# Kernel optimization log

Measured on AMD Instinct MI355X. Metric: run time of the kernel, lower is better.

Reference implementation:

```python
import jax, jax.numpy as jnp
import numpy as np

B, N, M, HW = 8, 256, 32, 32768
W_CLASS, W_CENTER, W_MASK, W_DICE = 2.0, 1.0, 5.0, 2.0


def setup_inputs() -> dict:
    key = jax.random.key(0)
    ks = jax.random.split(key, 6)
    sem_cls_prob = jax.random.uniform(ks[0], (B, N, 1), dtype=jnp.float32)
    center_dist = jax.random.uniform(ks[1], (B, N, M), dtype=jnp.float32)
    mask_heatmaps = jax.random.normal(ks[2], (B, HW, N), dtype=jnp.float32)
    # binary targets, as assumed by the dice/BCE cost math
    mask_tgt = jnp.round(jax.random.uniform(ks[3], (B, M, HW), dtype=jnp.float32))
    gt_plane_sem_cls_label = jax.random.randint(ks[4], (B, M), 0, 2).astype(jnp.int64)
    nactual_gt = jax.random.randint(ks[5], (B,), 1, M + 1).astype(jnp.int64)
    return {
        'sem_cls_prob': sem_cls_prob,
        'center_dist': center_dist,
        'mask_heatmaps': mask_heatmaps,
        'mask_tgt': mask_tgt,
        'gt_plane_sem_cls_label': gt_plane_sem_cls_label,
        'nactual_gt': nactual_gt,
    }


def _final_cost(sem_cls_prob, center_dist, mask_heatmaps, mask_tgt, labels):
    # class cost: -gathered prob from cat(1-p, p) -> [B, N, M]
    cls_cat = jnp.concatenate([1.0 - sem_cls_prob, sem_cls_prob], axis=-1)  # [B, N, 2]
    lbl = jnp.broadcast_to(labels[:, None, :], (B, N, M))
    class_mat = -jnp.take_along_axis(cls_cat, lbl, axis=2)

    x = jnp.swapaxes(mask_heatmaps, 1, 2)  # [B, N, HW] logits (mask_heatmaps[b].T)
    # BCE-with-logits: pos = softplus(-x) (target=1), neg = x + softplus(-x) (target=0)
    pos = jax.nn.softplus(-x)
    neg = x + pos
    cost_mask = (jnp.einsum('bnc,bmc->bnm', pos, mask_tgt)
                 + jnp.einsum('bnc,bmc->bnm', neg, 1.0 - mask_tgt)) / HW

    s = jax.nn.sigmoid(x)
    numerator = 2.0 * jnp.einsum('bnc,bmc->bnm', s, mask_tgt)
    denominator = s.sum(-1)[:, :, None] + mask_tgt.sum(-1)[:, None, :]
    cost_dice = 1.0 - (numerator + 1.0) / (denominator + 1.0)

    return (W_CLASS * class_mat + W_CENTER * center_dist
            + W_MASK * cost_mask + W_DICE * cost_dice)


def reference(sem_cls_prob, center_dist, mask_heatmaps, mask_tgt,
              gt_plane_sem_cls_label, nactual_gt):
    # nactual_gt only gates the (serial, CPU) Hungarian step, which is out of
    # kernel scope; the GPU-side math is the fused final cost matrix.
    return _final_cost(sem_cls_prob, center_dist, mask_heatmaps, mask_tgt,
                       gt_plane_sem_cls_label)
```

## Files before the change

### kernel.cpp

```cpp
#include <hip/hip_runtime.h>
#include <hip/hip_bf16.h>

#define NB   8
#define NN   256
#define NM   32
#define NHW  32768

#define CCH    4
#define CSLAB  (NHW / CCH)
#define NT     16
#define WPB    8
#define CW     (CSLAB / WPB)
#define ITERS  (CW / 32)

#define OFF_DXP  0
#define SZ_DXP   (CCH*NB*NT*512)
#define OFF_DSP  (OFF_DXP + SZ_DXP)
#define SZ_DSP   SZ_DXP
#define OFF_SNP  (OFF_DSP + SZ_DSP)
#define SZ_SNP   (CCH*NB*NN)
#define OFF_SSP  (OFF_SNP + SZ_SNP)
#define SZ_SSP   SZ_SNP
#define OFF_STGT (OFF_SSP + SZ_SSP)

typedef _Float16 half8 __attribute__((ext_vector_type(8)));
typedef float    f32x4 __attribute__((ext_vector_type(4)));

__global__ __launch_bounds__(256) void sum_tgt(const float* __restrict__ T,
                                               float* __restrict__ ws) {
    const int blk  = blockIdx.x;
    const int tid  = threadIdx.x;
    const int lane = tid & 63;
    const int wave = tid >> 6;
    const float* tp = T + (size_t)blk * NHW;

    float s = 0.f;
    for (int k = 0; k < NHW / (256 * 4); ++k) {
        float4 v = *(const float4*)(tp + (size_t)k * 1024 + tid * 4);
        s += (v.x + v.y) + (v.z + v.w);
    }
    s += __shfl_down(s, 32);
    s += __shfl_down(s, 16);
    s += __shfl_down(s, 8);
    s += __shfl_down(s, 4);
    s += __shfl_down(s, 2);
    s += __shfl_down(s, 1);

    __shared__ float r4[4];
    if (lane == 0) r4[wave] = s;
    __syncthreads();
    if (tid == 0) ws[OFF_STGT + blk] = (r4[0] + r4[1]) + (r4[2] + r4[3]);
}

__global__ __launch_bounds__(512, 4) void cost_main(
    const float* __restrict__ X,
    const float* __restrict__ T,
    float* __restrict__ ws) {
    const int blk  = blockIdx.x;
    const int b    = blk & 7;
    const int rest = blk >> 3;
    const int ch   = rest & 3;
    const int nt   = rest >> 2;

    const int tid  = threadIdx.x;
    const int wave = tid >> 6;
    const int lane = tid & 63;
    const int l16  = lane & 15;
    const int quad = lane >> 4;

    const int n0 = nt * 16;
    const int c0 = ch * CSLAB + wave * CW;

    const float* Xp  = X + ((size_t)b * NHW + c0 + quad * 8) * NN + n0 + l16;
    const float* T0p = T + ((size_t)b * NM + l16)      * NHW + c0 + quad * 8;
    const float* T1p = T + ((size_t)b * NM + l16 + 16) * NHW + c0 + quad * 8;

    f32x4 ax0 = {0.f, 0.f, 0.f, 0.f}, ax1 = {0.f, 0.f, 0.f, 0.f};
    f32x4 as0 = {0.f, 0.f, 0.f, 0.f}, as1 = {0.f, 0.f, 0.f, 0.f};
    float sneg = 0.f, ssig = 0.f;

    for (int it = 0; it < ITERS; ++it) {
        float xv[8];
#pragma unroll
        for (int j = 0; j < 8; ++j)
            xv[j] = Xp[(size_t)j * NN];

        float4 ta = *(const float4*)(T0p);
        float4 tb = *(const float4*)(T0p + 4);
        float4 tc = *(const float4*)(T1p);
        float4 td = *(const float4*)(T1p + 4);

        half8 hx, hs, ht0, ht1;
#pragma unroll
        for (int j = 0; j < 8; ++j) {
            float x = xv[j];
            float e = __expf(-fabsf(x));
            float r = __builtin_amdgcn_rcpf(1.f + e);
            float s = (x >= 0.f) ? r : 1.f - r;
            float pos = fmaxf(-x, 0.f) + __logf(1.f + e);
            sneg += x + pos;
            ssig += s;
            hx[j] = (_Float16)x;
            hs[j] = (_Float16)s;
        }
        ht0[0] = (_Float16)ta.x; ht0[1] = (_Float16)ta.y;
        ht0[2] = (_Float16)ta.z; ht0[3] = (_Float16)ta.w;
        ht0[4] = (_Float16)tb.x; ht0[5] = (_Float16)tb.y;
        ht0[6] = (_Float16)tb.z; ht0[7] = (_Float16)tb.w;
        ht1[0] = (_Float16)tc.x; ht1[1] = (_Float16)tc.y;
        ht1[2] = (_Float16)tc.z; ht1[3] = (_Float16)tc.w;
        ht1[4] = (_Float16)td.x; ht1[5] = (_Float16)td.y;
        ht1[6] = (_Float16)td.z; ht1[7] = (_Float16)td.w;

        ax0 = __builtin_amdgcn_mfma_f32_16x16x32_f16(hx, ht0, ax0, 0, 0, 0);
        ax1 = __builtin_amdgcn_mfma_f32_16x16x32_f16(hx, ht1, ax1, 0, 0, 0);
        as0 = __builtin_amdgcn_mfma_f32_16x16x32_f16(hs, ht0, as0, 0, 0, 0);
        as1 = __builtin_amdgcn_mfma_f32_16x16x32_f16(hs, ht1, as1, 0, 0, 0);

        Xp  += (size_t)32 * NN;
        T0p += 32;
        T1p += 32;
    }

    __shared__ float redx[512];
    __shared__ float reds[512];
    __shared__ float redn[16];
    __shared__ float redss[16];
    redx[tid] = 0.f;
    reds[tid] = 0.f;
    if (tid < 16) { redn[tid] = 0.f; redss[tid] = 0.f; }
    __syncthreads();

#pragma unroll
    for (int r = 0; r < 4; ++r) {
        const int row = quad * 4 + r;
        atomicAdd(&redx[row * 32 + l16],      ax0[r]);
        atomicAdd(&redx[row * 32 + l16 + 16], ax1[r]);
        atomicAdd(&reds[row * 32 + l16],      as0[r]);
        atomicAdd(&reds[row * 32 + l16 + 16], as1[r]);
    }
    sneg += __shfl_down(sneg, 32);
    sneg += __shfl_down(sneg, 16);
    ssig += __shfl_down(ssig, 32);
    ssig += __shfl_down(ssig, 16);
    if (lane < 16) {
        atomicAdd(&redn[l16], sneg);
        atomicAdd(&redss[l16], ssig);
    }
    __syncthreads();

    const size_t base = ((size_t)(ch * NB + b) * NT + nt);
    ws[OFF_DXP + base * 512 + tid] = redx[tid];
    ws[OFF_DSP + base * 512 + tid] = reds[tid];
    if (tid < 16) {
        ws[OFF_SNP + (ch * NB + b) * NN + n0 + tid] = redn[tid];
        ws[OFF_SSP + (ch * NB + b) * NN + n0 + tid] = redss[tid];
    }
}

__global__ __launch_bounds__(256) void cost_finalize(
    const float* __restrict__ P,
    const float* __restrict__ CD,
    const int*   __restrict__ LAB,
    const float* __restrict__ ws,
    float* __restrict__ out) {
    const int idx = blockIdx.x * 256 + threadIdx.x;
    const int m = idx & 31;
    const int n = (idx >> 5) & 255;
    const int b = idx >> 13;
    const int nt = n >> 4, nl = n & 15;

    float dx = 0.f, ds = 0.f, sn = 0.f, ss = 0.f;
#pragma unroll
    for (int ch = 0; ch < CCH; ++ch) {
        const size_t base = ((size_t)(ch * NB + b) * NT + nt) * 512 + nl * 32 + m;
        dx += ws[OFF_DXP + base];
        ds += ws[OFF_DSP + base];
        sn += ws[OFF_SNP + (ch * NB + b) * NN + n];
        ss += ws[OFF_SSP + (ch * NB + b) * NN + n];
    }
    const float st  = ws[OFF_STGT + b * NM + m];
    const float p   = P[b * NN + n];
    const int   lab = LAB[b * NM + m];
    const float cls = lab ? -p : (p - 1.f);

    const float cmask = (sn - dx) * (1.f / (float)NHW);
    const float dice  = 1.f - (2.f * ds + 1.f) / (ss + st + 1.f);

    out[idx] = 2.f * cls + CD[idx] + 5.f * cmask + 2.f * dice;
}

extern "C" void kernel_launch(void* const* d_in, const int* in_sizes, int n_in,
                              void* d_out, int out_size, void* d_ws, size_t ws_size,
                              hipStream_t stream) {
    const float* P   = (const float*)d_in[0];
    const float* CD  = (const float*)d_in[1];
    const float* X   = (const float*)d_in[2];
    const float* T   = (const float*)d_in[3];
    const int*   LAB = (const int*)d_in[4];
    float* out = (float*)d_out;
    float* ws  = (float*)d_ws;

    hipLaunchKernelGGL(sum_tgt, dim3(NB * NM), dim3(256), 0, stream, T, ws);
    hipLaunchKernelGGL(cost_main, dim3(NB * NT * CCH), dim3(512), 0, stream, X, T, ws);
    hipLaunchKernelGGL(cost_finalize, dim3((NB * NN * NM) / 256), dim3(256), 0, stream,
                       P, CD, LAB, ws, out);
}
```

Measured before the change: 433.6 us.

## Widen N tile to 64 to reuse target fragments and fuse target sum

Each block now covers 64 prediction rows instead of 16, so the converted target fragments are loaded once and reused across four MFMA column groups rather than re-read by sixteen separate N-tiles. The HW dimension is split into 16 chunks instead of 4 to keep the block count at 512. The separate target-sum kernel is removed and its row sums are computed inside the main loop, with the finalize kernel adding the per-chunk partials. The cost is more accumulator registers per thread, larger shared-memory reductions, and more partials for the finalize kernel to read.

After: 529.7 us. 22.2% more time.

```diff
diff --git a/kernel.cpp b/kernel.cpp
--- a/kernel.cpp
+++ b/kernel.cpp
@@ -6,61 +6,35 @@
 #define NM   32
 #define NHW  32768
 
-#define CCH    4
+#define NT4    4
+#define CCH    16
 #define CSLAB  (NHW / CCH)
-#define NT     16
 #define WPB    8
 #define CW     (CSLAB / WPB)
-#define ITERS  (CW / 32)
+#define KSTEPS (CW / 32)
 
 #define OFF_DXP  0
-#define SZ_DXP   (CCH*NB*NT*512)
+#define SZ_DXP   (CCH*NB*NT4*2048)
 #define OFF_DSP  (OFF_DXP + SZ_DXP)
-#define SZ_DSP   SZ_DXP
-#define OFF_SNP  (OFF_DSP + SZ_DSP)
+#define OFF_SNP  (OFF_DSP + SZ_DXP)
 #define SZ_SNP   (CCH*NB*NN)
 #define OFF_SSP  (OFF_SNP + SZ_SNP)
-#define SZ_SSP   SZ_SNP
-#define OFF_STGT (OFF_SSP + SZ_SSP)
+#define OFF_STGT (OFF_SSP + SZ_SNP)
 
 typedef _Float16 half8 __attribute__((ext_vector_type(8)));
 typedef float    f32x4 __attribute__((ext_vector_type(4)));
 
-__global__ __launch_bounds__(256) void sum_tgt(const float* __restrict__ T,
-                                               float* __restrict__ ws) {
-    const int blk  = blockIdx.x;
-    const int tid  = threadIdx.x;
-    const int lane = tid & 63;
-    const int wave = tid >> 6;
-    const float* tp = T + (size_t)blk * NHW;
-
-    float s = 0.f;
-    for (int k = 0; k < NHW / (256 * 4); ++k) {
-        float4 v = *(const float4*)(tp + (size_t)k * 1024 + tid * 4);
-        s += (v.x + v.y) + (v.z + v.w);
-    }
-    s += __shfl_down(s, 32);
-    s += __shfl_down(s, 16);
-    s += __shfl_down(s, 8);
-    s += __shfl_down(s, 4);
-    s += __shfl_down(s, 2);
-    s += __shfl_down(s, 1);
-
-    __shared__ float r4[4];
-    if (lane == 0) r4[wave] = s;
-    __syncthreads();
-    if (tid == 0) ws[OFF_STGT + blk] = (r4[0] + r4[1]) + (r4[2] + r4[3]);
-}
+#define MFMA16(a, b, c) __builtin_amdgcn_mfma_f32_16x16x32_f16(a, b, c, 0, 0, 0)
 
 __global__ __launch_bounds__(512, 4) void cost_main(
     const float* __restrict__ X,
     const float* __restrict__ T,
     float* __restrict__ ws) {
-    const int blk  = blockIdx.x;
-    const int b    = blk & 7;
-    const int rest = blk >> 3;
-    const int ch   = rest & 3;
-    const int nt   = rest >> 2;
+    const int blk = blockIdx.x;
+    const int b   = blk & 7;
+    const int rr  = blk >> 3;
+    const int ch  = rr & (CCH - 1);
+    const int nt4 = rr >> 4;
 
     const int tid  = threadIdx.x;
     const int wave = tid >> 6;
@@ -68,94 +42,117 @@
     const int l16  = lane & 15;
     const int quad = lane >> 4;
 
-    const int n0 = nt * 16;
+    const int n0 = nt4 * 64;
     const int c0 = ch * CSLAB + wave * CW;
 
     const float* Xp  = X + ((size_t)b * NHW + c0 + quad * 8) * NN + n0 + l16;
-    const float* T0p = T + ((size_t)b * NM + l16)      * NHW + c0 + quad * 8;
-    const float* T1p = T + ((size_t)b * NM + l16 + 16) * NHW + c0 + quad * 8;
-
-    f32x4 ax0 = {0.f, 0.f, 0.f, 0.f}, ax1 = {0.f, 0.f, 0.f, 0.f};
-    f32x4 as0 = {0.f, 0.f, 0.f, 0.f}, as1 = {0.f, 0.f, 0.f, 0.f};
-    float sneg = 0.f, ssig = 0.f;
-
-    for (int it = 0; it < ITERS; ++it) {
-        float xv[8];
-#pragma unroll
-        for (int j = 0; j < 8; ++j)
-            xv[j] = Xp[(size_t)j * NN];
-
+    const float* T0p = T + ((size_t)b * NM + l16) * NHW + c0 + quad * 8;
+    const float* T1p = T0p + (size_t)16 * NHW;
+
+    f32x4 ax0[4], ax1[4], as0[4], as1[4];
+#pragma unroll
+    for (int f = 0; f < 4; ++f) {
+        ax0[f] = f32x4{0.f, 0.f, 0.f, 0.f};
+        ax1[f] = f32x4{0.f, 0.f, 0.f, 0.f};
+        as0[f] = f32x4{0.f, 0.f, 0.f, 0.f};
+        as1[f] = f32x4{0.f, 0.f, 0.f, 0.f};
+    }
+    float sneg[4] = {0.f, 0.f, 0.f, 0.f};
+    float ssig[4] = {0.f, 0.f, 0.f, 0.f};
+    float ts0 = 0.f, ts1 = 0.f;
+
+    for (int ks = 0; ks < KSTEPS; ++ks) {
         float4 ta = *(const float4*)(T0p);
         float4 tb = *(const float4*)(T0p + 4);
         float4 tc = *(const float4*)(T1p);
         float4 td = *(const float4*)(T1p + 4);
-
-        half8 hx, hs, ht0, ht1;
-#pragma unroll
-        for (int j = 0; j < 8; ++j) {
-            float x = xv[j];
-            float e = __expf(-fabsf(x));
-            float r = __builtin_amdgcn_rcpf(1.f + e);
-            float s = (x >= 0.f) ? r : 1.f - r;
-            float pos = fmaxf(-x, 0.f) + __logf(1.f + e);
-            sneg += x + pos;
-            ssig += s;
-            hx[j] = (_Float16)x;
-            hs[j] = (_Float16)s;
-        }
-        ht0[0] = (_Float16)ta.x; ht0[1] = (_Float16)ta.y;
-        ht0[2] = (_Float16)ta.z; ht0[3] = (_Float16)ta.w;
-        ht0[4] = (_Float16)tb.x; ht0[5] = (_Float16)tb.y;
-        ht0[6] = (_Float16)tb.z; ht0[7] = (_Float16)tb.w;
-        ht1[0] = (_Float16)tc.x; ht1[1] = (_Float16)tc.y;
-        ht1[2] = (_Float16)tc.z; ht1[3] = (_Float16)tc.w;
-        ht1[4] = (_Float16)td.x; ht1[5] = (_Float16)td.y;
-        ht1[6] = (_Float16)td.z; ht1[7] = (_Float16)td.w;
-
-        ax0 = __builtin_amdgcn_mfma_f32_16x16x32_f16(hx, ht0, ax0, 0, 0, 0);
-        ax1 = __builtin_amdgcn_mfma_f32_16x16x32_f16(hx, ht1, ax1, 0, 0, 0);
-        as0 = __builtin_amdgcn_mfma_f32_16x16x32_f16(hs, ht0, as0, 0, 0, 0);
-        as1 = __builtin_amdgcn_mfma_f32_16x16x32_f16(hs, ht1, as1, 0, 0, 0);
-
+        half8 ht0 = {(_Float16)ta.x, (_Float16)ta.y, (_Float16)ta.z, (_Float16)ta.w,
+                     (_Float16)tb.x, (_Float16)tb.y, (_Float16)tb.z, (_Float16)tb.w};
+        half8 ht1 = {(_Float16)tc.x, (_Float16)tc.y, (_Float16)tc.z, (_Float16)tc.w,
+                     (_Float16)td.x, (_Float16)td.y, (_Float16)td.z, (_Float16)td.w};
+        ts0 += (ta.x + ta.y) + (ta.z + ta.w) + (tb.x + tb.y) + (tb.z + tb.w);
+        ts1 += (tc.x + tc.y) + (tc.z + tc.w) + (td.x + td.y) + (td.z + td.w);
+
+#pragma unroll
+        for (int f = 0; f < 4; ++f) {
+            float xv[8];
+#pragma unroll
+            for (int j = 0; j < 8; ++j)
+                xv[j] = Xp[(size_t)j * NN + f * 16];
+            half8 hx, hs;
+#pragma unroll
+            for (int j = 0; j < 8; ++j) {
+                float x = xv[j];
+                float e = __expf(-fabsf(x));
+                float rc = __builtin_amdgcn_rcpf(1.f + e);
+                float s  = (x >= 0.f) ? rc : 1.f - rc;
+                float pos = fmaxf(-x, 0.f) + __logf(1.f + e);
+                sneg[f] += x + pos;
+                ssig[f] += s;
+                hx[j] = (_Float16)x;
+                hs[j] = (_Float16)s;
+            }
+            ax0[f] = MFMA16(hx, ht0, ax0[f]);
+            ax1[f] = MFMA16(hx, ht1, ax1[f]);
+            as0[f] = MFMA16(hs, ht0, as0[f]);
+            as1[f] = MFMA16(hs, ht1, as1[f]);
+        }
         Xp  += (size_t)32 * NN;
         T0p += 32;
         T1p += 32;
     }
 
-    __shared__ float redx[512];
-    __shared__ float reds[512];
-    __shared__ float redn[16];
-    __shared__ float redss[16];
-    redx[tid] = 0.f;
-    reds[tid] = 0.f;
-    if (tid < 16) { redn[tid] = 0.f; redss[tid] = 0.f; }
+    __shared__ float redx[2048];
+    __shared__ float reds[2048];
+    __shared__ float redn[64];
+    __shared__ float redss[64];
+    __shared__ float redt[32];
+    for (int i = tid; i < 2048; i += 512) { redx[i] = 0.f; reds[i] = 0.f; }
+    if (tid < 64) { redn[tid] = 0.f; redss[tid] = 0.f; }
+    if (tid < 32) redt[tid] = 0.f;
     __syncthreads();
 
 #pragma unroll
-    for (int r = 0; r < 4; ++r) {
-        const int row = quad * 4 + r;
-        atomicAdd(&redx[row * 32 + l16],      ax0[r]);
-        atomicAdd(&redx[row * 32 + l16 + 16], ax1[r]);
-        atomicAdd(&reds[row * 32 + l16],      as0[r]);
-        atomicAdd(&reds[row * 32 + l16 + 16], as1[r]);
-    }
-    sneg += __shfl_down(sneg, 32);
-    sneg += __shfl_down(sneg, 16);
-    ssig += __shfl_down(ssig, 32);
-    ssig += __shfl_down(ssig, 16);
-    if (lane < 16) {
-        atomicAdd(&redn[l16], sneg);
-        atomicAdd(&redss[l16], ssig);
+    for (int f = 0; f < 4; ++f) {
+#pragma unroll
+        for (int r = 0; r < 4; ++r) {
+            const int row = f * 16 + quad * 4 + r;
+            atomicAdd(&redx[row * 32 + l16],      ax0[f][r]);
+            atomicAdd(&redx[row * 32 + l16 + 16], ax1[f][r]);
+            atomicAdd(&reds[row * 32 + l16],      as0[f][r]);
+            atomicAdd(&reds[row * 32 + l16 + 16], as1[f][r]);
+        }
+        float sn = sneg[f], ss = ssig[f];
+        sn += __shfl_xor(sn, 16); sn += __shfl_xor(sn, 32);
+        ss += __shfl_xor(ss, 16); ss += __shfl_xor(ss, 32);
+        if (lane < 16) {
+            atomicAdd(&redn[f * 16 + l16], sn);
+            atomicAdd(&redss[f * 16 + l16], ss);
+        }
+    }
+    {
+        float t0 = ts0, t1 = ts1;
+        t0 += __shfl_xor(t0, 16); t0 += __shfl_xor(t0, 32);
+        t1 += __shfl_xor(t1, 16); t1 += __shfl_xor(t1, 32);
+        if (lane < 16) {
+            atomicAdd(&redt[l16], t0);
+            atomicAdd(&redt[l16 + 16], t1);
+        }
     }
     __syncthreads();
 
-    const size_t base = ((size_t)(ch * NB + b) * NT + nt);
-    ws[OFF_DXP + base * 512 + tid] = redx[tid];
-    ws[OFF_DSP + base * 512 + tid] = reds[tid];
-    if (tid < 16) {
-        ws[OFF_SNP + (ch * NB + b) * NN + n0 + tid] = redn[tid];
-        ws[OFF_SSP + (ch * NB + b) * NN + n0 + tid] = redss[tid];
-    }
+    const size_t base = (((size_t)ch * NB + b) * NT4 + nt4) * 2048;
+    for (int i = tid; i < 2048; i += 512) {
+        ws[OFF_DXP + base + i] = redx[i];
+        ws[OFF_DSP + base + i] = reds[i];
+    }
+    if (tid < 64) {
+        const size_t sb = ((size_t)ch * NB + b) * NN + n0 + tid;
+        ws[OFF_SNP + sb] = redn[tid];
+        ws[OFF_SSP + sb] = redss[tid];
+    }
+    if (nt4 == 0 && tid < 32)
+        ws[OFF_STGT + ((size_t)ch * NB + b) * NM + tid] = redt[tid];
 }
 
 __global__ __launch_bounds__(256) void cost_finalize(
@@ -168,18 +165,18 @@
     const int m = idx & 31;
     const int n = (idx >> 5) & 255;
     const int b = idx >> 13;
-    const int nt = n >> 4, nl = n & 15;
-
-    float dx = 0.f, ds = 0.f, sn = 0.f, ss = 0.f;
+    const int nt4 = n >> 6, nl = n & 63;
+
+    float dx = 0.f, ds = 0.f, sn = 0.f, ss = 0.f, st = 0.f;
 #pragma unroll
     for (int ch = 0; ch < CCH; ++ch) {
-        const size_t base = ((size_t)(ch * NB + b) * NT + nt) * 512 + nl * 32 + m;
+        const size_t base = (((size_t)ch * NB + b) * NT4 + nt4) * 2048 + nl * 32 + m;
         dx += ws[OFF_DXP + base];
         ds += ws[OFF_DSP + base];
-        sn += ws[OFF_SNP + (ch * NB + b) * NN + n];
-        ss += ws[OFF_SSP + (ch * NB + b) * NN + n];
-    }
-    const float st  = ws[OFF_STGT + b * NM + m];
+        sn += ws[OFF_SNP + ((size_t)ch * NB + b) * NN + n];
+        ss += ws[OFF_SSP + ((size_t)ch * NB + b) * NN + n];
+        st += ws[OFF_STGT + ((size_t)ch * NB + b) * NM + m];
+    }
     const float p   = P[b * NN + n];
     const int   lab = LAB[b * NM + m];
     const float cls = lab ? -p : (p - 1.f);
@@ -201,8 +198,7 @@
     float* out = (float*)d_out;
     float* ws  = (float*)d_ws;
 
-    hipLaunchKernelGGL(sum_tgt, dim3(NB * NM), dim3(256), 0, stream, T, ws);
-    hipLaunchKernelGGL(cost_main, dim3(NB * NT * CCH), dim3(512), 0, stream, X, T, ws);
+    hipLaunchKernelGGL(cost_main, dim3(NT4 * CCH * NB), dim3(512), 0, stream, X, T, ws);
     hipLaunchKernelGGL(cost_finalize, dim3((NB * NN * NM) / 256), dim3(256), 0, stream,
                        P, CD, LAB, ws, out);
 }
```
